# Kernel tuning notes

Hardware: AMD Instinct MI355X
Metric: run time of the kernel (lower is better)

The kernel has to match this reference:

```python
import jax, jax.numpy as jnp
import numpy as np

GROUPS = 32
EPS = 1e-5


def group_norm(x, gamma, beta):
    # x: [B,H,W,C], channels_last, groups over channel dim (Keras GroupNormalization default)
    B, H, W, C = x.shape
    xg = x.reshape(B, H, W, GROUPS, C // GROUPS)
    mean = xg.mean(axis=(1, 2, 4), keepdims=True)
    var = xg.var(axis=(1, 2, 4), keepdims=True)
    xn = ((xg - mean) * jax.lax.rsqrt(var + EPS)).reshape(B, H, W, C)
    return xn * gamma + beta


def conv1x1(x, w, b):
    # 1x1 conv == per-pixel dense: [B,H,W,C] x [C,D] -> [B,H,W,D]
    return jnp.einsum('bhwc,cd->bhwd', x, w) + b


def setup_inputs() -> dict:
    key = jax.random.key(0)
    ks = jax.random.split(key, 10)
    C = 512
    s = 1.0 / np.sqrt(C)
    inp = {
        'x': jax.random.normal(ks[0], (2, 64, 64, C), dtype=jnp.float32),
        'gamma': jnp.ones((C,), jnp.float32),
        'beta': jnp.zeros((C,), jnp.float32),
        'wq': jax.random.normal(ks[1], (C, C), jnp.float32) * s,
        'bq': jnp.zeros((C,), jnp.float32),
        'wk': jax.random.normal(ks[2], (C, C), jnp.float32) * s,
        'bk': jnp.zeros((C,), jnp.float32),
        'wv': jax.random.normal(ks[3], (C, C), jnp.float32) * s,
        'bv': jnp.zeros((C,), jnp.float32),
        'wp': jax.random.normal(ks[4], (C, C), jnp.float32) * s,
        'bp': jnp.zeros((C,), jnp.float32),
    }
    return inp


def reference(x, gamma, beta, wq, bq, wk, bk, wv, bv, wp, bp):
    B, H, W, C = x.shape
    N = H * W
    xn = group_norm(x, gamma, beta)
    q = conv1x1(xn, wq, bq).reshape(B, N, C)
    k = conv1x1(xn, wk, bk).reshape(B, N, C)
    v = conv1x1(xn, wv, bv).reshape(B, N, C)
    scale = 1.0 / jnp.sqrt(jnp.asarray(C, x.dtype))
    scores = jnp.einsum('bnc,bmc->bnm', q, k) * scale  # [B,N,N]
    attn = jax.nn.softmax(scores, axis=-1)
    out = jnp.einsum('bnm,bmc->bnc', attn, v).reshape(B, H, W, C)
    return conv1x1(out, wp, bp) + x
```

## Files before the change

kernel.cpp:

```cpp
#include <hip/hip_runtime.h>
#include <hip/hip_fp16.h>

typedef _Float16 half_t;
typedef _Float16 half8 __attribute__((ext_vector_type(8)));
typedef float floatx4 __attribute__((ext_vector_type(4)));

static constexpr int BATCH = 2;
static constexpr int NSP = 4096;
static constexpr int CH = 512;
static constexpr int NQKV = 3 * CH;
static constexpr int KSPLIT = 4;

static constexpr size_t OFF_STATS = 0;
static constexpr size_t OFF_ROWSUM = 512;
static constexpr size_t OFF_PST = 33280;
static constexpr size_t OFF_WQKV = 196608;
static constexpr size_t WQKV_BYTES = (size_t)NQKV * CH * 2;
static constexpr size_t OFF_WP = OFF_WQKV + WQKV_BYTES;
static constexpr size_t WP_BYTES = (size_t)CH * CH * 2;
static constexpr size_t OFF_XN = OFF_WP + WP_BYTES;
static constexpr size_t XN_BYTES = (size_t)BATCH * NSP * CH * 2;
static constexpr size_t OFF_QKV = OFF_XN + XN_BYTES;
static constexpr size_t QKV_BYTES = (size_t)BATCH * NSP * NQKV * 2;
static constexpr size_t OFF_VT = OFF_QKV + QKV_BYTES;
static constexpr size_t OFF_AO = OFF_VT + XN_BYTES;
static constexpr size_t OFF_S = OFF_AO + XN_BYTES;
static constexpr size_t S_BYTES_1 = (size_t)NSP * NSP * 2;
static constexpr size_t OFF_PART = OFF_XN;

__device__ __forceinline__ void gld16(void* lds, const void* g) {
  __builtin_amdgcn_global_load_lds(
      (__attribute__((address_space(1))) void*)(g),
      (__attribute__((address_space(3))) void*)(lds),
      16, 0, 0);
}

#define VMCNT(n) asm volatile("s_waitcnt vmcnt(" #n ")" ::: "memory")
#define LGKM0()                                         \
  do {                                                  \
    asm volatile("s_waitcnt lgkmcnt(0)" ::: "memory");  \
    __builtin_amdgcn_sched_barrier(0);                  \
  } while (0)

__global__ __launch_bounds__(256) void gn_stats(const float* __restrict__ x,
                                                float* __restrict__ pst) {
  int b = blockIdx.y;
  int tid = (int)threadIdx.x;
  int g = ((tid * 4) & (CH - 1)) >> 4;
  const float* base = x + (long)b * NSP * CH + (long)blockIdx.x * 16 * CH + tid * 4;
  float s = 0.f, s2 = 0.f;
#pragma unroll
  for (int it = 0; it < 8; ++it) {
    floatx4 v = *(const floatx4*)(base + (long)it * 1024);
#pragma unroll
    for (int r = 0; r < 4; ++r) { s += v[r]; s2 += v[r] * v[r]; }
  }
  __shared__ float gs[32], gs2[32];
  if (tid < 32) { gs[tid] = 0.f; gs2[tid] = 0.f; }
  __syncthreads();
  atomicAdd(&gs[g], s);
  atomicAdd(&gs2[g], s2);
  __syncthreads();
  if (tid < 32) {
    long idx = ((long)(b * 256 + blockIdx.x) * 32 + tid) * 2;
    pst[idx] = gs[tid];
    pst[idx + 1] = gs2[tid];
  }
}

__global__ __launch_bounds__(256) void gn_finalize(const float* __restrict__ pst,
                                                   float* __restrict__ st,
                                                   float* __restrict__ rowsum) {
  int tid = (int)threadIdx.x;
  int bg = tid & 63;
  int p = tid >> 6;
  int b = bg >> 5, g = bg & 31;
  float s = 0.f, s2 = 0.f;
  for (int j = 0; j < 64; ++j) {
    int chunk = p * 64 + j;
    long idx = ((long)(b * 256 + chunk) * 32 + g) * 2;
    s += pst[idx];
    s2 += pst[idx + 1];
  }
  __shared__ float rs[64][4], rs2[64][4];
  rs[bg][p] = s;
  rs2[bg][p] = s2;
  __syncthreads();
  if (tid < 64) {
    float ts = rs[tid][0] + rs[tid][1] + rs[tid][2] + rs[tid][3];
    float ts2 = rs2[tid][0] + rs2[tid][1] + rs2[tid][2] + rs2[tid][3];
    const float inv = 1.f / 65536.f;
    float mean = ts * inv;
    float var = ts2 * inv - mean * mean;
    st[tid * 2] = mean;
    st[tid * 2 + 1] = rsqrtf(var + 1e-5f);
  }
  floatx4* rz = (floatx4*)rowsum;
#pragma unroll
  for (int j = 0; j < 8; ++j)
    rz[tid + j * 256] = floatx4{0.f, 0.f, 0.f, 0.f};
}

__global__ __launch_bounds__(256) void gn_apply(const float* __restrict__ x,
                                                const float* __restrict__ st,
                                                const float* __restrict__ gamma,
                                                const float* __restrict__ beta,
                                                half_t* __restrict__ xn) {
  long i = ((long)blockIdx.x * 256 + threadIdx.x) * 8;
  int c = (int)(i & (CH - 1));
  int b = (int)(i >> 21);
  int g = c >> 4;
  float mean = st[((b << 5) + g) * 2];
  float rstd = st[((b << 5) + g) * 2 + 1];
  floatx4 a = *(const floatx4*)(x + i);
  floatx4 d = *(const floatx4*)(x + i + 4);
  half8 o;
#pragma unroll
  for (int r = 0; r < 4; ++r) {
    o[r]     = (half_t)((a[r] - mean) * rstd * gamma[c + r] + beta[c + r]);
    o[r + 4] = (half_t)((d[r] - mean) * rstd * gamma[c + r + 4] + beta[c + r + 4]);
  }
  *(half8*)(xn + i) = o;
}

__global__ __launch_bounds__(256) void transpose_w(
    const float* __restrict__ w0, const float* __restrict__ w1,
    const float* __restrict__ w2, const float* __restrict__ w3,
    half_t* __restrict__ o0, half_t* __restrict__ o1,
    half_t* __restrict__ o2, half_t* __restrict__ o3) {
  const float* w; half_t* o;
  switch (blockIdx.z) {
    case 0: w = w0; o = o0; break;
    case 1: w = w1; o = o1; break;
    case 2: w = w2; o = o2; break;
    default: w = w3; o = o3; break;
  }
  __shared__ float t[32][33];
  int d0 = blockIdx.x * 32, c0 = blockIdx.y * 32;
  int tx = threadIdx.x & 31, ty = threadIdx.x >> 5;
#pragma unroll
  for (int i = 0; i < 4; ++i)
    t[ty + i * 8][tx] = w[(long)(c0 + ty + i * 8) * CH + d0 + tx];
  __syncthreads();
#pragma unroll
  for (int i = 0; i < 4; ++i) {
    int d = ty + i * 8;
    o[(long)(d0 + d) * CH + c0 + tx] = (half_t)t[tx][d];
  }
}

__global__ __launch_bounds__(256) void transpose_v(const half_t* __restrict__ v,
                                                   half_t* __restrict__ vt) {
  __shared__ half_t t[32][33];
  int b = blockIdx.z;
  int d0 = blockIdx.x * 32, n0 = blockIdx.y * 32;
  int tx = threadIdx.x & 31, ty = threadIdx.x >> 5;
  const half_t* vb = v + (long)b * NSP * NQKV;
  half_t* ob = vt + (long)b * NSP * CH;
#pragma unroll
  for (int i = 0; i < 4; ++i)
    t[ty + i * 8][tx] = vb[(long)(n0 + ty + i * 8) * NQKV + d0 + tx];
  __syncthreads();
#pragma unroll
  for (int i = 0; i < 4; ++i) {
    int d = ty + i * 8;
    ob[(long)(d0 + d) * NSP + n0 + tx] = t[tx][d];
  }
}

template <int BM, int BN, int BK, int EPI, int SWZ, int KSP, typename OutT>
__global__ __launch_bounds__(256) void gemm_nt(
    const half_t* __restrict__ X, const half_t* __restrict__ Y,
    OutT* __restrict__ Co, const float* __restrict__ b0,
    const float* __restrict__ b1, const float* __restrict__ b2,
    const float* __restrict__ resid, float* __restrict__ rowsum,
    int M, int N, int K, int ldx, int ldy, int ldc,
    long xbs, long ybs, long cbs, float scale) {
  constexpr int SM = BM / 32;
  constexpr int SN = BN / 32;
  constexpr int ROWS = BM + BN;
  constexpr int CPR = BK / 8;
  constexpr int RPW = 64 / CPR;
  constexpr int ROUNDS = (ROWS * BK * 2) / 4096;
  constexpr int KSTEPS = BK / 32;
  static_assert(BM % (4 * RPW) == 0, "no As/Bs straddle within a round");
  __shared__ __align__(16) half_t Sh[ROWS * BK];

  const int zb = blockIdx.z / KSP;
  const int ks = blockIdx.z % KSP;
  int bx, by;
  if (SWZ == 1) {
    int lin = (int)(blockIdx.x + gridDim.x * blockIdx.y);
    int wmt = 256 / (int)gridDim.x;
    by = wmt * (lin >> 8) + ((lin & 255) % wmt);
    bx = (lin & 255) / wmt;
  } else if (SWZ == 2) {
    by = blockIdx.x;
    bx = blockIdx.y;
  } else {
    bx = blockIdx.x;
    by = blockIdx.y;
  }

  const half_t* Xb = X + (long)zb * xbs + (long)ks * K;
  const half_t* Yb = Y + (long)zb * ybs + (long)ks * K;
  OutT* Cb = Co + (long)blockIdx.z * cbs;

  const int m0 = by * BM;
  const int n0 = bx * BN;
  const int tid = (int)threadIdx.x;
  const int wave = tid >> 6;
  const int lane = tid & 63;
  const int quad = lane >> 4;
  const int l16 = lane & 15;
  const int wm = wave >> 1;
  const int wn = wave & 1;

  floatx4 acc[SM][SN] = {};

  const int srow = lane / CPR;
  const int schunk = lane % CPR;
  const char* Xc = (const char*)Xb;

  int soff[ROUNDS];
#pragma unroll
  for (int r = 0; r < ROUNDS; ++r) {
    int row = r * (4 * RPW) + wave * RPW + srow;
    int gchunk = schunk ^ (row & (CPR - 1));
    const char* p = (row < BM)
        ? (const char*)(Xb + (long)(m0 + row) * ldx)
        : (const char*)(Yb + (long)(n0 + row - BM) * ldy);
    soff[r] = (int)(p + gchunk * 16 - Xc);
  }

  int offA[SM], offB[SN];
#pragma unroll
  for (int i = 0; i < SM; ++i) {
    int m = wm * (BM / 2) + i * 16 + l16;
    int cc = quad ^ (m & (CPR - 1));
    offA[i] = (m * BK + cc * 8) * 2;
  }
#pragma unroll
  for (int j = 0; j < SN; ++j) {
    int n = wn * (BN / 2) + j * 16 + l16;
    int cc = quad ^ (n & (CPR - 1));
    offB[j] = (BM * BK + n * BK + cc * 8) * 2;
  }

  for (int k0 = 0; k0 < K; k0 += BK) {
#pragma unroll
    for (int r = 0; r < ROUNDS; ++r) {
      gld16((char*)Sh + (r * 4 + wave) * 1024, Xc + (long)soff[r]);
      soff[r] += BK * 2;
    }
    __syncthreads();

#pragma unroll
    for (int kk = 0; kk < KSTEPS; ++kk) {
      const int kx = kk << 6;
      half8 af[SM], bf[SN];
#pragma unroll
      for (int i = 0; i < SM; ++i)
        af[i] = *(const half8*)((const char*)Sh + (offA[i] ^ kx));
#pragma unroll
      for (int j = 0; j < SN; ++j)
        bf[j] = *(const half8*)((const char*)Sh + (offB[j] ^ kx));
#pragma unroll
      for (int i = 0; i < SM; ++i)
#pragma unroll
        for (int j = 0; j < SN; ++j)
          acc[i][j] = __builtin_amdgcn_mfma_f32_16x16x32_f16(af[i], bf[j], acc[i][j], 0, 0, 0);
    }
    __syncthreads();
  }

#pragma unroll
  for (int i = 0; i < SM; ++i) {
    int gmb = m0 + wm * (BM / 2) + i * 16 + quad * 4;
#pragma unroll
    for (int j = 0; j < SN; ++j) {
      int gn = n0 + wn * (BN / 2) + j * 16 + l16;
      float bias = 0.f, sc = 1.f;
      if (EPI == 1) {
        if (gn < CH) { bias = b0[gn]; sc = scale; }
        else if (gn < 2 * CH) { bias = b1[gn - CH]; }
        else { bias = b2[gn - 2 * CH]; }
      } else if (EPI == 2) {
        bias = b0[gn];
      }
#pragma unroll
      for (int r = 0; r < 4; ++r) {
        long idx = (long)(gmb + r) * ldc + gn;
        float v = acc[i][j][r];
        if (EPI == 1) v = (v + bias) * sc;
        if (EPI == 2) v = v + bias + resid[idx];
        Cb[idx] = (OutT)v;
      }
    }
  }
}

template <int EPI, int KSP, int SW, typename OutT>
__global__ __launch_bounds__(512, 2) void gemm8p(
    const half_t* __restrict__ X, const half_t* __restrict__ Y,
    OutT* __restrict__ Co, float* __restrict__ rowsum,
    int K, int ldx, int ldy, int ldc, long xbs, long ybs, long cbs) {
  __shared__ __align__(16) char smem[131072];
  const int zb = (int)blockIdx.z / KSP;
  const int ks = (int)blockIdx.z % KSP;
  int by, bx;
  if (SW == 1) {
    const int lin = (int)(blockIdx.x + (blockIdx.y << 4));
    const int xcd = lin & 7;
    const int kk2 = lin >> 3;
    by = (xcd & 3) * 4 + (kk2 & 3);
    bx = (xcd >> 2) * 8 + (kk2 >> 2);
  } else {
    by = (int)blockIdx.x;
    bx = (int)blockIdx.y;
  }
  const int m0 = by * 256;
  const int n0 = bx * 256;
  const int tid = (int)threadIdx.x;
  const int w = tid >> 6;
  const int l = tid & 63;
  const int quad = l >> 4;
  const int l16 = l & 15;
  const int wm = w >> 2;
  const int wn = w & 3;

  const half_t* Xb = X + (long)zb * xbs + (long)ks * K;
  const half_t* Yb = Y + (long)zb * ybs + (long)ks * K;
  OutT* Cb = Co + (long)blockIdx.z * cbs;
  const char* Xc = (const char*)Xb;

  int soff[8];
  {
    const int lr = l >> 3;
    const int g = (l & 7) ^ (lr & 7);
#pragma unroll
    for (int r = 0; r < 8; ++r) {
      const int R = (r * 8 + w) * 8 + lr;
      const char* p = (R < 256)
          ? (const char*)(Xb + (long)(m0 + R) * ldx)
          : (const char*)(Yb + (long)(n0 + R - 256) * ldy);
      soff[r] = (int)(p + g * 16 - Xc);
    }
  }

  int offA[8], offB[4];
#pragma unroll
  for (int i = 0; i < 8; ++i) {
    const int m = wm * 128 + i * 16 + l16;
    offA[i] = m * 128 + ((quad ^ (m & 7)) << 4);
  }
#pragma unroll
  for (int j = 0; j < 4; ++j) {
    const int n = wn * 64 + j * 16 + l16;
    offB[j] = 32768 + n * 128 + ((quad ^ (n & 7)) << 4);
  }

  floatx4 acc[8][4] = {};

#pragma unroll
  for (int r = 0; r < 8; ++r) {
    gld16(smem + (r * 8 + w) * 1024, Xc + (long)soff[r]);
    soff[r] += 128;
  }
  {
    constexpr int pr[6] = {4, 5, 6, 7, 0, 2};
#pragma unroll
    for (int t = 0; t < 6; ++t) {
      gld16(smem + 65536 + (pr[t] * 8 + w) * 1024, Xc + (long)soff[pr[t]]);
      soff[pr[t]] += 128;
    }
  }
  VMCNT(6);
  __builtin_amdgcn_s_barrier();

  const int NI = K >> 7;
  half8 bf[4][2];
  for (int it = 0; it < NI; ++it) {
    const bool last = (it == NI - 1);
    constexpr int sr0[8] = {1, 4, 6, 0, 1, 4, 6, 0};
    constexpr int sr1[8] = {3, 5, 7, 2, 3, 5, 7, 2};
    constexpr int spar[8] = {1, 0, 0, 0, 0, 1, 1, 1};
    constexpr int hoist[8] = {1, 1, 1, 0, 1, 0, 1, 0};
    half8 af[2][2];
#pragma unroll
    for (int ph = 0; ph < 8; ++ph) {
      const int q = ph & 3;
      const char* bb = smem + (ph >> 2) * 65536;
      if (q == 0) {
#pragma unroll
        for (int j = 0; j < 4; ++j)
#pragma unroll
          for (int kk = 0; kk < 2; ++kk)
            bf[j][kk] = *(const half8*)(bb + (offB[j] ^ (kk << 6)));
#pragma unroll
        for (int i2 = 0; i2 < 2; ++i2)
#pragma unroll
          for (int kk = 0; kk < 2; ++kk)
            af[i2][kk] = *(const half8*)(bb + (offA[i2] ^ (kk << 6)));
      } else if (ph == 6) {
#pragma unroll
        for (int i2 = 0; i2 < 2; ++i2)
#pragma unroll
          for (int kk = 0; kk < 2; ++kk)
            af[i2][kk] = *(const half8*)(bb + (offA[q * 2 + i2] ^ (kk << 6)));
      }
      if (ph == 0 || !last) {
        const int r0 = sr0[ph], r1 = sr1[ph];
        char* db = smem + spar[ph] * 65536;
        gld16(db + (r0 * 8 + w) * 1024, Xc + (long)soff[r0]);
        soff[r0] += 128;
        gld16(db + (r1 * 8 + w) * 1024, Xc + (long)soff[r1]);
        soff[r1] += 128;
      }
      LGKM0();
      __builtin_amdgcn_s_setprio(1);
#pragma unroll
      for (int i2 = 0; i2 < 2; ++i2)
#pragma unroll
        for (int j = 0; j < 4; ++j)
#pragma unroll
          for (int kk = 0; kk < 2; ++kk)
            acc[q * 2 + i2][j] = __builtin_amdgcn_mfma_f32_16x16x32_f16(
                af[i2][kk], bf[j][kk], acc[q * 2 + i2][j], 0, 0, 0);
      __builtin_amdgcn_s_setprio(0);
      if (ph == 3) {
        if (last) { VMCNT(2); } else { VMCNT(8); }
      } else if (ph == 5) {
        if (last) { VMCNT(0); } else { VMCNT(10); }
      }
      if (hoist[ph]) {
        const int np = ph + 1;
        const int nq = np & 3;
        const char* nb = smem + ((np >> 2) & 1) * 65536;
#pragma unroll
        for (int i2 = 0; i2 < 2; ++i2)
#pragma unroll
          for (int kk = 0; kk < 2; ++kk)
            af[i2][kk] = *(const half8*)(nb + (offA[nq * 2 + i2] ^ (kk << 6)));
        __builtin_amdgcn_sched_barrier(0);
      }
      if (ph == 7) {
        if (!last) { VMCNT(6); }
      }
      __builtin_amdgcn_s_barrier();
    }
  }

#pragma unroll
  for (int i = 0; i < 8; ++i) {
    const int gmb = m0 + wm * 128 + i * 16 + quad * 4;
    float rs[4] = {0.f, 0.f, 0.f, 0.f};
#pragma unroll
    for (int j = 0; j < 4; ++j) {
      const int gn = n0 + wn * 64 + j * 16 + l16;
#pragma unroll
      for (int r = 0; r < 4; ++r) {
        long idx = (long)(gmb + r) * ldc + gn;
        float v = acc[i][j][r];
        if (EPI == 3) { v = __expf(v); rs[r] += v; }
        Cb[idx] = (OutT)v;
      }
    }
    if (EPI == 3) {
#pragma unroll
      for (int r = 0; r < 4; ++r) {
        float v = rs[r];
        v += __shfl_xor(v, 1);
        v += __shfl_xor(v, 2);
        v += __shfl_xor(v, 4);
        v += __shfl_xor(v, 8);
        if (l16 == 0) atomicAdd(&rowsum[(long)zb * NSP + gmb + r], v);
      }
    }
  }
}

__global__ __launch_bounds__(256) void pv_combine(const half_t* __restrict__ part,
                                                  const float* __restrict__ rowsum,
                                                  half_t* __restrict__ ao) {
  const long bNC = (long)NSP * CH;
  long i = ((long)blockIdx.x * 256 + threadIdx.x) * 8;
  int b = (int)(i >> 21);
  long inner = i & ((1L << 21) - 1);
  float inv = 1.f / rowsum[i >> 9];
  float s[8] = {};
#pragma unroll
  for (int ks = 0; ks < KSPLIT; ++ks) {
    half8 h = *(const half8*)(part + ((long)(b * KSPLIT + ks)) * bNC + inner);
#pragma unroll
    for (int r = 0; r < 8; ++r) s[r] += (float)h[r];
  }
  half8 o;
#pragma unroll
  for (int r = 0; r < 8; ++r) o[r] = (half_t)(s[r] * inv);
  *(half8*)(ao + i) = o;
}

extern "C" void kernel_launch(void* const* d_in, const int* in_sizes, int n_in,
                              void* d_out, int out_size, void* d_ws, size_t ws_size,
                              hipStream_t stream) {
  const float* x = (const float*)d_in[0];
  const float* gamma = (const float*)d_in[1];
  const float* beta = (const float*)d_in[2];
  const float* wq = (const float*)d_in[3];
  const float* bq = (const float*)d_in[4];
  const float* wk = (const float*)d_in[5];
  const float* bk = (const float*)d_in[6];
  const float* wv = (const float*)d_in[7];
  const float* bv = (const float*)d_in[8];
  const float* wp = (const float*)d_in[9];
  const float* bp = (const float*)d_in[10];
  float* out = (float*)d_out;
  char* ws = (char*)d_ws;

  float* st = (float*)(ws + OFF_STATS);
  float* rsum = (float*)(ws + OFF_ROWSUM);
  float* pst = (float*)(ws + OFF_PST);
  half_t* wqkvT = (half_t*)(ws + OFF_WQKV);
  half_t* wpT = (half_t*)(ws + OFF_WP);
  half_t* xn = (half_t*)(ws + OFF_XN);
  half_t* qkv = (half_t*)(ws + OFF_QKV);
  half_t* vt = (half_t*)(ws + OFF_VT);
  half_t* ao = (half_t*)(ws + OFF_AO);
  half_t* S = (half_t*)(ws + OFF_S);
  half_t* part = (half_t*)(ws + OFF_PART);

  half_t* q = qkv;
  half_t* k = qkv + CH;
  half_t* v = qkv + 2 * CH;

  const float scale = 0.044194173824159216f;
  const long bQKV = (long)NSP * NQKV;
  const long bNC = (long)NSP * CH;
  const long bNN = (long)NSP * NSP;

  gn_stats<<<dim3(256, BATCH), 256, 0, stream>>>(x, pst);
  gn_finalize<<<1, 256, 0, stream>>>(pst, st, rsum);
  gn_apply<<<2048, 256, 0, stream>>>(x, st, gamma, beta, xn);
  transpose_w<<<dim3(16, 16, 4), 256, 0, stream>>>(
      wq, wk, wv, wp, wqkvT, wqkvT + (size_t)CH * CH, wqkvT + 2 * (size_t)CH * CH, wpT);

  gemm_nt<128, 128, 64, 1, 2, 1, half_t><<<dim3(BATCH * NSP / 128, NQKV / 128, 1), 256, 0, stream>>>(
      xn, wqkvT, qkv, bq, bk, bv, nullptr, nullptr, BATCH * NSP, NQKV, CH,
      CH, CH, NQKV, 0, 0, 0, scale);
  transpose_v<<<dim3(16, 128, BATCH), 256, 0, stream>>>(v, vt);

  bool full = ws_size >= OFF_S + 2 * S_BYTES_1;
  if (full) {
    gemm8p<3, 1, 1, half_t><<<dim3(16, 16, BATCH), 512, 0, stream>>>(
        q, k, S, rsum, CH, NQKV, NQKV, NSP, bQKV, bQKV, bNN);
    gemm8p<0, KSPLIT, 0, half_t><<<dim3(NSP / 256, CH / 256, BATCH * KSPLIT), 512, 0, stream>>>(
        S, vt, part, nullptr, NSP / KSPLIT, NSP, NSP, CH, bNN, bNC, bNC);
    pv_combine<<<2048, 256, 0, stream>>>(part, rsum, ao);
  } else {
    for (int bb = 0; bb < BATCH; ++bb) {
      gemm8p<3, 1, 1, half_t><<<dim3(16, 16, 1), 512, 0, stream>>>(
          q + bb * bQKV, k + bb * bQKV, S, rsum + bb * NSP, CH,
          NQKV, NQKV, NSP, 0, 0, 0);
      gemm8p<0, KSPLIT, 0, half_t><<<dim3(NSP / 256, CH / 256, KSPLIT), 512, 0, stream>>>(
          S, vt + bb * bNC, part + (long)bb * KSPLIT * bNC, nullptr,
          NSP / KSPLIT, NSP, NSP, CH, 0, 0, bNC);
    }
    pv_combine<<<2048, 256, 0, stream>>>(part, rsum, ao);
  }
  gemm_nt<64, 64, 128, 2, 2, 1, float><<<dim3(BATCH * NSP / 64, CH / 64, 1), 256, 0, stream>>>(
      ao, wpT, out, bp, nullptr, nullptr, x, nullptr, BATCH * NSP, CH, CH,
      CH, CH, CH, 0, 0, 0, 1.f);
}
```

Baseline: 236.3 us.

## Fuse prep kernels, prefetch Q/K into L2, remap PV grid per XCD

Merges the group-norm statistics kernel and the weight transpose into one launch to save a kernel launch. The V transpose kernel now also loads slices of Q and K, with XCD-aware row assignment, so they are likely resident in each XCD's L2 before the QK^T GEMM runs. The PV split-K GEMM uses a new 1D grid mapping that keeps related tiles on the same XCD to improve L2 reuse of S and V^T. The prefetch adds extra global reads to the transpose, and correctness depends on the new index mapping covering every tile.

Result: no change. 237.6 us (+0.6%).

```diff
diff --git a/kernel.cpp b/kernel.cpp
--- a/kernel.cpp
+++ b/kernel.cpp
@@ -42,29 +42,60 @@
     __builtin_amdgcn_sched_barrier(0);                  \
   } while (0)
 
-__global__ __launch_bounds__(256) void gn_stats(const float* __restrict__ x,
-                                                float* __restrict__ pst) {
-  int b = blockIdx.y;
-  int tid = (int)threadIdx.x;
-  int g = ((tid * 4) & (CH - 1)) >> 4;
-  const float* base = x + (long)b * NSP * CH + (long)blockIdx.x * 16 * CH + tid * 4;
-  float s = 0.f, s2 = 0.f;
-#pragma unroll
-  for (int it = 0; it < 8; ++it) {
-    floatx4 v = *(const floatx4*)(base + (long)it * 1024);
-#pragma unroll
-    for (int r = 0; r < 4; ++r) { s += v[r]; s2 += v[r] * v[r]; }
-  }
+__global__ __launch_bounds__(256) void prep(
+    const float* __restrict__ x, float* __restrict__ pst,
+    const float* __restrict__ w0, const float* __restrict__ w1,
+    const float* __restrict__ w2, const float* __restrict__ w3,
+    half_t* __restrict__ o0, half_t* __restrict__ o1,
+    half_t* __restrict__ o2, half_t* __restrict__ o3) {
   __shared__ float gs[32], gs2[32];
-  if (tid < 32) { gs[tid] = 0.f; gs2[tid] = 0.f; }
-  __syncthreads();
-  atomicAdd(&gs[g], s);
-  atomicAdd(&gs2[g], s2);
-  __syncthreads();
-  if (tid < 32) {
-    long idx = ((long)(b * 256 + blockIdx.x) * 32 + tid) * 2;
-    pst[idx] = gs[tid];
-    pst[idx + 1] = gs2[tid];
+  __shared__ float tw[32][33];
+  const int bid = (int)blockIdx.x;
+  const int tid = (int)threadIdx.x;
+  if (bid < 512) {
+    const int b = bid >> 8;
+    const int chunk = bid & 255;
+    int g = ((tid * 4) & (CH - 1)) >> 4;
+    const float* base = x + (long)b * NSP * CH + (long)chunk * 16 * CH + tid * 4;
+    float s = 0.f, s2 = 0.f;
+#pragma unroll
+    for (int it = 0; it < 8; ++it) {
+      floatx4 v = *(const floatx4*)(base + (long)it * 1024);
+#pragma unroll
+      for (int r = 0; r < 4; ++r) { s += v[r]; s2 += v[r] * v[r]; }
+    }
+    if (tid < 32) { gs[tid] = 0.f; gs2[tid] = 0.f; }
+    __syncthreads();
+    atomicAdd(&gs[g], s);
+    atomicAdd(&gs2[g], s2);
+    __syncthreads();
+    if (tid < 32) {
+      long idx = ((long)(b * 256 + chunk) * 32 + tid) * 2;
+      pst[idx] = gs[tid];
+      pst[idx + 1] = gs2[tid];
+    }
+  } else {
+    const int t = bid - 512;
+    const int wz = t >> 8;
+    const int r = t & 255;
+    const float* w; half_t* o;
+    switch (wz) {
+      case 0: w = w0; o = o0; break;
+      case 1: w = w1; o = o1; break;
+      case 2: w = w2; o = o2; break;
+      default: w = w3; o = o3; break;
+    }
+    int d0 = (r & 15) * 32, c0 = (r >> 4) * 32;
+    int tx = tid & 31, ty = tid >> 5;
+#pragma unroll
+    for (int i = 0; i < 4; ++i)
+      tw[ty + i * 8][tx] = w[(long)(c0 + ty + i * 8) * CH + d0 + tx];
+    __syncthreads();
+#pragma unroll
+    for (int i = 0; i < 4; ++i) {
+      int d = ty + i * 8;
+      o[(long)(d0 + d) * CH + c0 + tx] = (half_t)tw[tx][d];
+    }
   }
 }
 
@@ -123,38 +154,29 @@
   *(half8*)(xn + i) = o;
 }
 
-__global__ __launch_bounds__(256) void transpose_w(
-    const float* __restrict__ w0, const float* __restrict__ w1,
-    const float* __restrict__ w2, const float* __restrict__ w3,
-    half_t* __restrict__ o0, half_t* __restrict__ o1,
-    half_t* __restrict__ o2, half_t* __restrict__ o3) {
-  const float* w; half_t* o;
-  switch (blockIdx.z) {
-    case 0: w = w0; o = o0; break;
-    case 1: w = w1; o = o1; break;
-    case 2: w = w2; o = o2; break;
-    default: w = w3; o = o3; break;
-  }
-  __shared__ float t[32][33];
-  int d0 = blockIdx.x * 32, c0 = blockIdx.y * 32;
-  int tx = threadIdx.x & 31, ty = threadIdx.x >> 5;
-#pragma unroll
-  for (int i = 0; i < 4; ++i)
-    t[ty + i * 8][tx] = w[(long)(c0 + ty + i * 8) * CH + d0 + tx];
-  __syncthreads();
-#pragma unroll
-  for (int i = 0; i < 4; ++i) {
-    int d = ty + i * 8;
-    o[(long)(d0 + d) * CH + c0 + tx] = (half_t)t[tx][d];
-  }
-}
-
 __global__ __launch_bounds__(256) void transpose_v(const half_t* __restrict__ v,
-                                                   half_t* __restrict__ vt) {
+                                                   half_t* __restrict__ vt,
+                                                   const half_t* __restrict__ qkv) {
   __shared__ half_t t[32][33];
+  const int tid = (int)threadIdx.x;
+  const int lin = (int)(blockIdx.x + gridDim.x * (blockIdx.y + gridDim.y * blockIdx.z));
+  const int xcd = lin & 7;
+  const int wi = lin >> 3;
+
+  {
+    int row = (xcd & 3) * 1024 + wi * 2 + (tid >> 7);
+    const long* p = (const long*)((const char*)qkv + (long)row * 3072 + (tid & 127) * 8);
+    long qa = *p;
+    int krow = (xcd >> 2) * 2048 + wi * 4 + (tid >> 6);
+    const floatx4* kp = (const floatx4*)((const char*)qkv + 1024 + (long)krow * 3072 + (tid & 63) * 16);
+    floatx4 ka = *kp;
+    asm volatile("" :: "v"((int)qa), "v"((int)(qa >> 32)),
+                 "v"(ka[0]), "v"(ka[1]), "v"(ka[2]), "v"(ka[3]));
+  }
+
   int b = blockIdx.z;
   int d0 = blockIdx.x * 32, n0 = blockIdx.y * 32;
-  int tx = threadIdx.x & 31, ty = threadIdx.x >> 5;
+  int tx = tid & 31, ty = tid >> 5;
   const half_t* vb = v + (long)b * NSP * NQKV;
   half_t* ob = vt + (long)b * NSP * CH;
 #pragma unroll
@@ -306,18 +328,28 @@
     OutT* __restrict__ Co, float* __restrict__ rowsum,
     int K, int ldx, int ldy, int ldc, long xbs, long ybs, long cbs) {
   __shared__ __align__(16) char smem[131072];
-  const int zb = (int)blockIdx.z / KSP;
-  const int ks = (int)blockIdx.z % KSP;
-  int by, bx;
+  int by, bx, zb, ks;
   if (SW == 1) {
     const int lin = (int)(blockIdx.x + (blockIdx.y << 4));
     const int xcd = lin & 7;
-    const int kk2 = lin >> 3;
-    by = (xcd & 3) * 4 + (kk2 & 3);
-    bx = (xcd >> 2) * 8 + (kk2 >> 2);
+    const int k2 = lin >> 3;
+    by = (xcd & 3) * 4 + (k2 & 3);
+    bx = (xcd >> 2) * 8 + (k2 >> 2);
+    zb = (int)blockIdx.z / KSP;
+    ks = (int)blockIdx.z % KSP;
+  } else if (SW == 2) {
+    const int xcd = (int)blockIdx.x & 7;
+    const int s = (int)blockIdx.x >> 3;
+    const int c = xcd * 2 + (s >> 4);
+    by = s & 15;
+    bx = c & 1;
+    ks = (c >> 1) & 3;
+    zb = c >> 3;
   } else {
     by = (int)blockIdx.x;
     bx = (int)blockIdx.y;
+    zb = (int)blockIdx.z / KSP;
+    ks = (int)blockIdx.z % KSP;
   }
   const int m0 = by * 256;
   const int n0 = bx * 256;
@@ -331,7 +363,7 @@
 
   const half_t* Xb = X + (long)zb * xbs + (long)ks * K;
   const half_t* Yb = Y + (long)zb * ybs + (long)ks * K;
-  OutT* Cb = Co + (long)blockIdx.z * cbs;
+  OutT* Cb = Co + ((long)(zb * KSP + ks)) * cbs;
   const char* Xc = (const char*)Xb;
 
   int soff[8];
@@ -539,22 +571,21 @@
   const long bNC = (long)NSP * CH;
   const long bNN = (long)NSP * NSP;
 
-  gn_stats<<<dim3(256, BATCH), 256, 0, stream>>>(x, pst);
+  prep<<<1536, 256, 0, stream>>>(x, pst, wq, wk, wv, wp,
+      wqkvT, wqkvT + (size_t)CH * CH, wqkvT + 2 * (size_t)CH * CH, wpT);
   gn_finalize<<<1, 256, 0, stream>>>(pst, st, rsum);
   gn_apply<<<2048, 256, 0, stream>>>(x, st, gamma, beta, xn);
-  transpose_w<<<dim3(16, 16, 4), 256, 0, stream>>>(
-      wq, wk, wv, wp, wqkvT, wqkvT + (size_t)CH * CH, wqkvT + 2 * (size_t)CH * CH, wpT);
 
   gemm_nt<128, 128, 64, 1, 2, 1, half_t><<<dim3(BATCH * NSP / 128, NQKV / 128, 1), 256, 0, stream>>>(
       xn, wqkvT, qkv, bq, bk, bv, nullptr, nullptr, BATCH * NSP, NQKV, CH,
       CH, CH, NQKV, 0, 0, 0, scale);
-  transpose_v<<<dim3(16, 128, BATCH), 256, 0, stream>>>(v, vt);
+  transpose_v<<<dim3(16, 128, BATCH), 256, 0, stream>>>(v, vt, qkv);
 
   bool full = ws_size >= OFF_S + 2 * S_BYTES_1;
   if (full) {
     gemm8p<3, 1, 1, half_t><<<dim3(16, 16, BATCH), 512, 0, stream>>>(
         q, k, S, rsum, CH, NQKV, NQKV, NSP, bQKV, bQKV, bNN);
-    gemm8p<0, KSPLIT, 0, half_t><<<dim3(NSP / 256, CH / 256, BATCH * KSPLIT), 512, 0, stream>>>(
+    gemm8p<0, KSPLIT, 2, half_t><<<dim3(256, 1, 1), 512, 0, stream>>>(
         S, vt, part, nullptr, NSP / KSPLIT, NSP, NSP, CH, bNN, bNC, bNC);
     pv_combine<<<2048, 256, 0, stream>>>(part, rsum, ao);
   } else {
```
